# Optimization experiments

Measured on AMD Instinct MI355X. Metric: run time of the kernel, lower is better.

The kernel has to match this reference:

```python
import jax, jax.numpy as jnp
import numpy as np

B, P, G, C = 64, 5000, 300, 20   # images, preds/img, gt/img, num classes
INPUT_SIZE = 512.0
IOU_THRESH = 0.5


def setup_inputs() -> dict:
    key = jax.random.key(0)
    k1, k2, k3, k4, k5, k6, k7 = jax.random.split(key, 7)
    # predictions: [x1,y1,x2,y2,score,cls], boxes normalized to [0,1]
    pxy = jax.random.uniform(k1, (B, P, 2), minval=0.0, maxval=0.8)
    pwh = jax.random.uniform(k2, (B, P, 2), minval=0.02, maxval=0.2)
    score = jax.random.uniform(k3, (B, P, 1))
    pcls = jax.random.randint(k4, (B, P, 1), 0, C).astype(jnp.float32)
    output = jnp.concatenate([pxy, pxy + pwh, score, pcls], axis=-1)
    # ground truth: [x1,y1,x2,y2,cls]
    txy = jax.random.uniform(k5, (B, G, 2), minval=0.0, maxval=0.8)
    twh = jax.random.uniform(k6, (B, G, 2), minval=0.02, maxval=0.2)
    tcls = jax.random.randint(k7, (B, G, 1), 0, C).astype(jnp.float32)
    labels = jnp.concatenate([txy, txy + twh, tcls], axis=-1)
    return {"output": output, "labels": labels}


def reference(output, labels):
    scale = jnp.array([INPUT_SIZE, INPUT_SIZE, INPUT_SIZE, INPUT_SIZE], dtype=output.dtype)

    def match_image(preds, targets):  # preds [P,6], targets [G,5]
        tcls = targets[:, 4]
        tboxes = targets[:, :4] * scale                     # [G,4]
        tarea = (tboxes[:, 2] - tboxes[:, 0]) * (tboxes[:, 3] - tboxes[:, 1])

        def step(detected, pred):
            pbox = pred[:4] * scale
            lt = jnp.maximum(pbox[:2], tboxes[:, :2])       # [G,2]
            rb = jnp.minimum(pbox[2:], tboxes[:, 2:])
            wh = jnp.clip(rb - lt, 0.0)
            inter = wh[:, 0] * wh[:, 1]
            parea = (pbox[2] - pbox[0]) * (pbox[3] - pbox[1])
            ious = inter / (parea + tarea - inter)          # [G]
            cls_mask = tcls == pred[5]
            masked = jnp.where(cls_mask, ious, -1.0)
            bi = jnp.argmax(masked)                          # greedy argmax over same-class gt
            match = ((pred[4] > 0)
                     & jnp.any(cls_mask)
                     & (masked[bi] > IOU_THRESH)
                     & (~detected[bi]))                      # sequential dedup
            detected = detected.at[bi].set(detected[bi] | match)
            return detected, match

        _, correct = jax.lax.scan(step, jnp.zeros(tboxes.shape[0], dtype=bool), preds)
        return correct                                       # [P] bool

    correct = jax.vmap(match_image)(output, labels).astype(output.dtype)  # [B,P]
    # stats: (correct flag, score, predicted class) per prediction; tcls per image
    stats = jnp.stack([correct, output[:, :, 4], output[:, :, 5]], axis=-1)  # [B,P,3]
    tcls = labels[:, :, 4]                                                    # [B,G]
    return stats, tcls
```

## Files before the change

### kernel.cpp

```cpp
#include <hip/hip_runtime.h>
#include <cstdint>

#define B 64
#define P 5000
#define G 300
#define C 20
#define SCALE_F 512.0f
#define IOU_TH 0.5f
#define NSPLIT 8
#define PCHUNK ((P + NSPLIT - 1) / NSPLIT)
#define NTA 512
#define SPT ((PCHUNK + NTA - 1) / NTA)
#define NCHUNK ((G + 63) / 64)
#define SENT 0x7FFFFFFF

#pragma clang fp contract(off)

__global__ __launch_bounds__(NTA, 4) void match_kernel(
    const float* __restrict__ preds,
    const float* __restrict__ labels,
    int* __restrict__ blockfp,
    float* __restrict__ out_stats,
    float* __restrict__ out_tcls)
{
    const int s = blockIdx.x;
    const int b = blockIdx.y;
    const int tid = threadIdx.x;

    __shared__ float4 sb[G];
    __shared__ float  sa[G];
    __shared__ short  ssi[G];
    __shared__ short  cls_s[G];
    __shared__ int    chist[NCHUNK][C];
    __shared__ int    cnt[C];
    __shared__ int    so[C + 1];
    __shared__ int    pcnt[C];
    __shared__ int    firstp[G];
    __shared__ unsigned short psorted[PCHUNK];

    const float* lab = labels + (size_t)b * G * 5;
    const float* prd = preds + (size_t)b * P * 6;
    const int pbase = s * PCHUNK;
    const int pend = (pbase + PCHUNK < P) ? pbase + PCHUNK : P;
    const int npred = pend - pbase;

    if (tid < NCHUNK * C) ((int*)chist)[tid] = 0;
    if (tid < C) pcnt[tid] = 0;
    if (tid < G) {
        float cf = lab[tid * 5 + 4];
        cls_s[tid] = (short)(int)cf;
        firstp[tid] = SENT;
        if (s == 0) out_tcls[(size_t)b * G + tid] = cf;
    }
    __syncthreads();

    if (tid < G) atomicAdd(&chist[tid >> 6][cls_s[tid]], 1);
    int myc[SPT];
    #pragma unroll
    for (int k = 0; k < SPT; ++k) {
        myc[k] = -1;
        int p = pbase + k * NTA + tid;
        if (p < pend) {
            float2 sc = *reinterpret_cast<const float2*>(prd + (size_t)p * 6 + 4);
            int c = (int)sc.y;
            myc[k] = c;
            atomicAdd(&pcnt[c], 1);
            size_t ip3 = ((size_t)b * P + p) * 3;
            out_stats[ip3 + 0] = 0.0f;
            out_stats[ip3 + 1] = sc.x;
            out_stats[ip3 + 2] = sc.y;
        }
    }
    __syncthreads();

    if (tid < C) {
        int run = 0;
        #pragma unroll
        for (int w = 0; w < NCHUNK; ++w) {
            int v = chist[w][tid]; chist[w][tid] = run; run += v;
        }
        cnt[tid] = run;
    }
    if (tid == 64) {
        int a = 0;
        for (int c = 0; c < C; ++c) { int v = pcnt[c]; pcnt[c] = a; a += v; }
    }
    __syncthreads();

    if (tid == 0) {
        int a = 0;
        for (int c = 0; c < C; ++c) { so[c] = a; a += cnt[c]; }
        so[C] = a;
    }
    __syncthreads();

    if (tid < NCHUNK * 64) {
        int c = (tid < G) ? (int)cls_s[tid] : -1;
        unsigned long long mymask = 0;
        #pragma unroll
        for (int cc = 0; cc < C; ++cc) {
            unsigned long long m = __ballot(c == cc);
            if (c == cc) mymask = m;
        }
        if (tid < G) {
            int lane = tid & 63;
            int rank = chist[tid >> 6][c]
                     + __popcll(mymask & ((1ull << lane) - 1));
            int pos = so[c] + rank;
            float x1 = lab[tid * 5 + 0] * SCALE_F;
            float y1 = lab[tid * 5 + 1] * SCALE_F;
            float x2 = lab[tid * 5 + 2] * SCALE_F;
            float y2 = lab[tid * 5 + 3] * SCALE_F;
            sb[pos] = make_float4(x1, y1, x2, y2);
            sa[pos] = (x2 - x1) * (y2 - y1);
            ssi[pos] = (short)tid;
        }
    }
    #pragma unroll
    for (int k = 0; k < SPT; ++k) {
        int p = pbase + k * NTA + tid;
        if (p < pend) {
            int pos = atomicAdd(&pcnt[myc[k]], 1);
            psorted[pos] = (unsigned short)p;
        }
    }
    __syncthreads();

    #pragma unroll
    for (int k = 0; k < SPT; ++k) {
        int slot = k * NTA + tid;
        if (slot >= npred) continue;
        int p = psorted[slot];
        const float* pr = prd + (size_t)p * 6;
        float2 q0 = *reinterpret_cast<const float2*>(pr);
        float2 q1 = *reinterpret_cast<const float2*>(pr + 2);
        float2 q2 = *reinterpret_cast<const float2*>(pr + 4);
        float px1 = q0.x * SCALE_F;
        float py1 = q0.y * SCALE_F;
        float px2 = q1.x * SCALE_F;
        float py2 = q1.y * SCALE_F;
        float score = q2.x;
        int c = (int)q2.y;
        float parea = (px2 - px1) * (py2 - py1);

        int lo = so[c], hi = so[c + 1];
        float best = -1.0f;
        int bi = -1;
        for (int j = lo; j < hi; ++j) {
            float4 tb = sb[j];
            float lx = fmaxf(px1, tb.x);
            float ly = fmaxf(py1, tb.y);
            float rx = fminf(px2, tb.z);
            float ry = fminf(py2, tb.w);
            float w = fmaxf(rx - lx, 0.0f);
            float h = fmaxf(ry - ly, 0.0f);
            float inter = w * h;
            float uni = (parea + sa[j]) - inter;
            float iou = inter / uni;
            if (iou > best) { best = iou; bi = ssi[j]; }
        }

        bool eligible = (score > 0.0f) && (hi > lo) && (best > IOU_TH);
        if (eligible) atomicMin(&firstp[bi], p);
    }
    __syncthreads();

    if (tid < G)
        blockfp[((size_t)b * NSPLIT + s) * G + tid] = firstp[tid];
}

__global__ __launch_bounds__(512) void resolve_kernel(
    const int* __restrict__ blockfp,
    float* __restrict__ out_stats)
{
    const int b = blockIdx.x;
    const int t = threadIdx.x;
    if (t >= G) return;

    const int* fp = blockfp + (size_t)b * NSPLIT * G + t;
    int m = fp[0];
    #pragma unroll
    for (int s = 1; s < NSPLIT; ++s) m = min(m, fp[s * G]);

    if (m != SENT)
        out_stats[((size_t)b * P + m) * 3] = 1.0f;
}

extern "C" void kernel_launch(void* const* d_in, const int* in_sizes, int n_in,
                              void* d_out, int out_size, void* d_ws, size_t ws_size,
                              hipStream_t stream) {
    const float* output = (const float*)d_in[0];
    const float* labels = (const float*)d_in[1];

    float* out_stats = (float*)d_out;
    float* out_tcls  = (float*)d_out + (size_t)B * P * 3;

    int* blockfp = (int*)d_ws;

    dim3 grid(NSPLIT, B);
    match_kernel<<<grid, NTA, 0, stream>>>(output, labels, blockfp,
                                           out_stats, out_tcls);
    resolve_kernel<<<dim3(B), 512, 0, stream>>>(blockfp, out_stats);
}
```

Baseline: 70.31 us.

## Replace atomic counting sort with ballot-based ranking and stage predictions in LDS

Replaces the shared-memory atomicAdd class histograms and serial prefix sums with per-wave ballot/popcount histograms plus a shuffle-based scan. This removes two block barriers and the single-thread scan loops. Prediction rows for the block's chunk are copied into LDS once, so the sorted-order pass reads LDS instead of scattered global memory. The price is about 15KB more shared memory per block, which may reduce occupancy, and more ballot work per thread.

```diff
diff --git a/kernel.cpp b/kernel.cpp
--- a/kernel.cpp
+++ b/kernel.cpp
@@ -10,7 +10,9 @@
 #define NSPLIT 8
 #define PCHUNK ((P + NSPLIT - 1) / NSPLIT)
 #define NTA 512
+#define NWAVE (NTA / 64)
 #define SPT ((PCHUNK + NTA - 1) / NTA)
+#define NPCH (SPT * NWAVE)
 #define NCHUNK ((G + 63) / 64)
 #define SENT 0x7FFFFFFF
 
@@ -26,15 +28,16 @@
     const int s = blockIdx.x;
     const int b = blockIdx.y;
     const int tid = threadIdx.x;
-
+    const int lane = tid & 63;
+    const int w = tid >> 6;
+
+    __shared__ float  plds[PCHUNK * 6];
     __shared__ float4 sb[G];
     __shared__ float  sa[G];
     __shared__ short  ssi[G];
-    __shared__ short  cls_s[G];
     __shared__ int    chist[NCHUNK][C];
-    __shared__ int    cnt[C];
+    __shared__ int    phist[NPCH][C];
     __shared__ int    so[C + 1];
-    __shared__ int    pcnt[C];
     __shared__ int    firstp[G];
     __shared__ unsigned short psorted[PCHUNK];
 
@@ -44,84 +47,111 @@
     const int pend = (pbase + PCHUNK < P) ? pbase + PCHUNK : P;
     const int npred = pend - pbase;
 
-    if (tid < NCHUNK * C) ((int*)chist)[tid] = 0;
-    if (tid < C) pcnt[tid] = 0;
-    if (tid < G) {
-        float cf = lab[tid * 5 + 4];
-        cls_s[tid] = (short)(int)cf;
-        firstp[tid] = SENT;
-        if (s == 0) out_tcls[(size_t)b * G + tid] = cf;
-    }
-    __syncthreads();
-
-    if (tid < G) atomicAdd(&chist[tid >> 6][cls_s[tid]], 1);
+    if (tid < G) firstp[tid] = SENT;
+
+    float tx1 = 0, ty1 = 0, tx2 = 0, ty2 = 0;
+    int tc = -1;
+    unsigned long long tmask = 0;
+    if (tid < NCHUNK * 64) {
+        if (tid < G) {
+            tx1 = lab[tid * 5 + 0];
+            ty1 = lab[tid * 5 + 1];
+            tx2 = lab[tid * 5 + 2];
+            ty2 = lab[tid * 5 + 3];
+            float cf = lab[tid * 5 + 4];
+            tc = (int)cf;
+            if (s == 0) out_tcls[(size_t)b * G + tid] = cf;
+        }
+        #pragma unroll
+        for (int cc = 0; cc < C; ++cc) {
+            unsigned long long m = __ballot(tc == cc);
+            if (tc == cc) tmask = m;
+            if (lane == cc) chist[w][cc] = __popcll(m);
+        }
+    }
+
+    for (int i = tid; i < npred * 6; i += NTA)
+        plds[i] = prd[(size_t)pbase * 6 + i];
+
     int myc[SPT];
+    unsigned long long pmask[SPT];
     #pragma unroll
     for (int k = 0; k < SPT; ++k) {
         myc[k] = -1;
+        pmask[k] = 0;
         int p = pbase + k * NTA + tid;
         if (p < pend) {
             float2 sc = *reinterpret_cast<const float2*>(prd + (size_t)p * 6 + 4);
-            int c = (int)sc.y;
-            myc[k] = c;
-            atomicAdd(&pcnt[c], 1);
+            myc[k] = (int)sc.y;
             size_t ip3 = ((size_t)b * P + p) * 3;
             out_stats[ip3 + 0] = 0.0f;
             out_stats[ip3 + 1] = sc.x;
             out_stats[ip3 + 2] = sc.y;
         }
-    }
-    __syncthreads();
-
-    if (tid < C) {
+        #pragma unroll
+        for (int cc = 0; cc < C; ++cc) {
+            unsigned long long m = __ballot(myc[k] == cc);
+            if (myc[k] == cc) pmask[k] = m;
+            if (lane == cc) phist[k * NWAVE + w][cc] = __popcll(m);
+        }
+    }
+    __syncthreads();
+
+    if (tid < 64) {
         int run = 0;
-        #pragma unroll
-        for (int w = 0; w < NCHUNK; ++w) {
-            int v = chist[w][tid]; chist[w][tid] = run; run += v;
-        }
-        cnt[tid] = run;
-    }
-    if (tid == 64) {
-        int a = 0;
-        for (int c = 0; c < C; ++c) { int v = pcnt[c]; pcnt[c] = a; a += v; }
-    }
-    __syncthreads();
-
-    if (tid == 0) {
-        int a = 0;
-        for (int c = 0; c < C; ++c) { so[c] = a; a += cnt[c]; }
-        so[C] = a;
-    }
-    __syncthreads();
-
-    if (tid < NCHUNK * 64) {
-        int c = (tid < G) ? (int)cls_s[tid] : -1;
-        unsigned long long mymask = 0;
-        #pragma unroll
-        for (int cc = 0; cc < C; ++cc) {
-            unsigned long long m = __ballot(c == cc);
-            if (c == cc) mymask = m;
-        }
-        if (tid < G) {
-            int lane = tid & 63;
-            int rank = chist[tid >> 6][c]
-                     + __popcll(mymask & ((1ull << lane) - 1));
-            int pos = so[c] + rank;
-            float x1 = lab[tid * 5 + 0] * SCALE_F;
-            float y1 = lab[tid * 5 + 1] * SCALE_F;
-            float x2 = lab[tid * 5 + 2] * SCALE_F;
-            float y2 = lab[tid * 5 + 3] * SCALE_F;
-            sb[pos] = make_float4(x1, y1, x2, y2);
-            sa[pos] = (x2 - x1) * (y2 - y1);
-            ssi[pos] = (short)tid;
-        }
+        if (lane < C) {
+            #pragma unroll
+            for (int u = 0; u < NCHUNK; ++u) {
+                int t = chist[u][lane]; chist[u][lane] = run; run += t;
+            }
+        }
+        int v = (lane < C) ? run : 0;
+        #pragma unroll
+        for (int d = 1; d < 32; d <<= 1) {
+            int o = __shfl_up(v, d);
+            if (lane >= d) v += o;
+        }
+        if (lane < C) so[lane + 1] = v;
+        if (lane == 0) so[0] = 0;
+    } else if (tid < 128) {
+        int run = 0;
+        if (lane < C) {
+            #pragma unroll
+            for (int u = 0; u < NPCH; ++u) {
+                int t = phist[u][lane]; phist[u][lane] = run; run += t;
+            }
+        }
+        int v = (lane < C) ? run : 0;
+        #pragma unroll
+        for (int d = 1; d < 32; d <<= 1) {
+            int o = __shfl_up(v, d);
+            if (lane >= d) v += o;
+        }
+        int excl = v - run;
+        if (lane < C) {
+            #pragma unroll
+            for (int u = 0; u < NPCH; ++u) phist[u][lane] += excl;
+        }
+    }
+    __syncthreads();
+
+    if (tid < G) {
+        int rank = chist[w][tc] + __popcll(tmask & ((1ull << lane) - 1));
+        int pos = so[tc] + rank;
+        float x1 = tx1 * SCALE_F;
+        float y1 = ty1 * SCALE_F;
+        float x2 = tx2 * SCALE_F;
+        float y2 = ty2 * SCALE_F;
+        sb[pos] = make_float4(x1, y1, x2, y2);
+        sa[pos] = (x2 - x1) * (y2 - y1);
+        ssi[pos] = (short)tid;
     }
     #pragma unroll
     for (int k = 0; k < SPT; ++k) {
-        int p = pbase + k * NTA + tid;
-        if (p < pend) {
-            int pos = atomicAdd(&pcnt[myc[k]], 1);
-            psorted[pos] = (unsigned short)p;
+        if (myc[k] >= 0) {
+            int pos = phist[k * NWAVE + w][myc[k]]
+                    + __popcll(pmask[k] & ((1ull << lane) - 1));
+            psorted[pos] = (unsigned short)(k * NTA + tid);
         }
     }
     __syncthreads();
@@ -130,11 +160,11 @@
     for (int k = 0; k < SPT; ++k) {
         int slot = k * NTA + tid;
         if (slot >= npred) continue;
-        int p = psorted[slot];
-        const float* pr = prd + (size_t)p * 6;
-        float2 q0 = *reinterpret_cast<const float2*>(pr);
-        float2 q1 = *reinterpret_cast<const float2*>(pr + 2);
-        float2 q2 = *reinterpret_cast<const float2*>(pr + 4);
+        int li = psorted[slot];
+        const float* pp = &plds[li * 6];
+        float2 q0 = *reinterpret_cast<const float2*>(pp);
+        float2 q1 = *reinterpret_cast<const float2*>(pp + 2);
+        float2 q2 = *reinterpret_cast<const float2*>(pp + 4);
         float px1 = q0.x * SCALE_F;
         float py1 = q0.y * SCALE_F;
         float px2 = q1.x * SCALE_F;
@@ -152,16 +182,16 @@
             float ly = fmaxf(py1, tb.y);
             float rx = fminf(px2, tb.z);
             float ry = fminf(py2, tb.w);
-            float w = fmaxf(rx - lx, 0.0f);
-            float h = fmaxf(ry - ly, 0.0f);
-            float inter = w * h;
+            float wd = fmaxf(rx - lx, 0.0f);
+            float ht = fmaxf(ry - ly, 0.0f);
+            float inter = wd * ht;
             float uni = (parea + sa[j]) - inter;
             float iou = inter / uni;
             if (iou > best) { best = iou; bi = ssi[j]; }
         }
 
         bool eligible = (score > 0.0f) && (hi > lo) && (best > IOU_TH);
-        if (eligible) atomicMin(&firstp[bi], p);
+        if (eligible) atomicMin(&firstp[bi], pbase + li);
     }
     __syncthreads();
 
```

Result: slower. 73.87 us (+5.1%).
